# Performance work log

Measured on AMD Instinct MI355X. Metric: run time of the kernel, lower is better.

Reference implementation:

```python
import jax, jax.numpy as jnp
import numpy as np

B, D_IMG, D_NUM, P = 16384, 2048, 256, 128

def setup_inputs() -> dict:
    key = jax.random.key(0)
    ks = jax.random.split(key, 12)
    s = lambda d: 1.0 / np.sqrt(d)
    return {
        "img_feat": jax.random.normal(ks[0], (B, D_IMG), jnp.float32),
        "num_feat": jax.random.normal(ks[1], (B, D_NUM), jnp.float32),
        "Wi1": jax.random.uniform(ks[2], (D_IMG, P), jnp.float32, -s(D_IMG), s(D_IMG)),
        "bi1": jax.random.uniform(ks[3], (P,), jnp.float32, -s(D_IMG), s(D_IMG)),
        "Wi2": jax.random.uniform(ks[4], (P, P), jnp.float32, -s(P), s(P)),
        "bi2": jax.random.uniform(ks[5], (P,), jnp.float32, -s(P), s(P)),
        "Wn1": jax.random.uniform(ks[6], (D_NUM, P), jnp.float32, -s(D_NUM), s(D_NUM)),
        "bn1": jax.random.uniform(ks[7], (P,), jnp.float32, -s(D_NUM), s(D_NUM)),
        "Wn2": jax.random.uniform(ks[8], (P, P), jnp.float32, -s(P), s(P)),
        "bn2": jax.random.uniform(ks[9], (P,), jnp.float32, -s(P), s(P)),
        "log_temp": jnp.asarray(np.log(0.1), jnp.float32),
    }

def _mlp(x, W1, b1, W2, b2):
    h = jax.nn.relu(x @ W1 + b1)
    return h @ W2 + b2

def _l2norm(x, eps=1e-12):
    # matches F.normalize(dim=1): x / max(||x||, eps)
    n = jnp.sqrt(jnp.sum(x * x, axis=1, keepdims=True))
    return x / jnp.maximum(n, eps)

def reference(img_feat, num_feat, Wi1, bi1, Wi2, bi2, Wn1, bn1, Wn2, bn2, log_temp):
    temp = jnp.exp(log_temp)
    ip = _l2norm(_mlp(img_feat, Wi1, bi1, Wi2, bi2))  # [B, P]
    npj = _l2norm(_mlp(num_feat, Wn1, bn1, Wn2, bn2))  # [B, P]
    logits = (ip @ npj.T) / temp                        # [B, B]
    # symmetric cross-entropy with labels = arange(B): targets on the diagonal
    lse_rows = jax.nn.logsumexp(logits, axis=1)  # i2n
    lse_cols = jax.nn.logsumexp(logits, axis=0)  # n2i (logits.T rows)
    diag = jnp.diagonal(logits)
    loss_i2n = jnp.mean(lse_rows - diag)
    loss_n2i = jnp.mean(lse_cols - diag)
    return (loss_i2n + loss_n2i) * 0.5
```

## Files before the change

### kernel.cpp

```cpp
#include <hip/hip_runtime.h>
#include <hip/hip_bf16.h>

typedef __bf16 bf16_t;
typedef __bf16 bf16x8 __attribute__((ext_vector_type(8)));
typedef float f32x4 __attribute__((ext_vector_type(4)));

#define NB 16384
#define NSPLIT 16
#define CG (NB / NSPLIT)
#define BNT 64
#define NT (CG / BNT)

__device__ inline bf16x8 ld8(const bf16_t* p) { return *(const bf16x8*)p; }

__device__ inline void gload_lds16(const bf16_t* g, bf16_t* l) {
  __builtin_amdgcn_global_load_lds(
      (const __attribute__((address_space(1))) unsigned int*)g,
      (__attribute__((address_space(3))) unsigned int*)l, 16, 0, 0);
}

__global__ void prep(const float* __restrict__ img, const float* __restrict__ num,
                     const float* __restrict__ Wi1, const float* __restrict__ Wn1,
                     const float* __restrict__ Wi2, const float* __restrict__ Wn2,
                     bf16_t* __restrict__ imgb, bf16_t* __restrict__ numb,
                     bf16_t* __restrict__ Wi1t, bf16_t* __restrict__ Wn1t,
                     bf16_t* __restrict__ Wi2t, bf16_t* __restrict__ Wn2t,
                     float* __restrict__ lossacc, int nimg, int nnum) {
  int b = blockIdx.x;
  if (b < nimg) {
    int base = b * 8192;
#pragma unroll
    for (int i = 0; i < 4; i++) {
      int e = base + (threadIdx.x + i * 256) * 8;
      int row = e >> 11, k = e & 2047;
      float4 f0 = *(const float4*)(img + e);
      float4 f1 = *(const float4*)(img + e + 4);
      bf16x8 v;
      v[0]=(bf16_t)f0.x; v[1]=(bf16_t)f0.y; v[2]=(bf16_t)f0.z; v[3]=(bf16_t)f0.w;
      v[4]=(bf16_t)f1.x; v[5]=(bf16_t)f1.y; v[6]=(bf16_t)f1.z; v[7]=(bf16_t)f1.w;
      *(bf16x8*)(imgb + (size_t)row * 2048 + (k ^ ((row & 7) << 3))) = v;
    }
    return;
  }
  b -= nimg;
  if (b < nnum) {
    int base = b * 8192;
#pragma unroll
    for (int i = 0; i < 4; i++) {
      int e = base + (threadIdx.x + i * 256) * 8;
      int row = e >> 8, k = e & 255;
      float4 f0 = *(const float4*)(num + e);
      float4 f1 = *(const float4*)(num + e + 4);
      bf16x8 v;
      v[0]=(bf16_t)f0.x; v[1]=(bf16_t)f0.y; v[2]=(bf16_t)f0.z; v[3]=(bf16_t)f0.w;
      v[4]=(bf16_t)f1.x; v[5]=(bf16_t)f1.y; v[6]=(bf16_t)f1.z; v[7]=(bf16_t)f1.w;
      *(bf16x8*)(numb + (size_t)row * 256 + (k ^ ((row & 7) << 3))) = v;
    }
    return;
  }
  b -= nnum;
  if (b < 1280) {
    int idx = b * 256 + threadIdx.x;
    if (idx < 262144) { int k = idx >> 7, n = idx & 127;
      Wi1t[n * 2048 + (k ^ ((n & 7) << 3))] = (bf16_t)Wi1[idx]; return; }
    idx -= 262144;
    if (idx < 32768) { int k = idx >> 7, n = idx & 127;
      Wn1t[n * 256 + (k ^ ((n & 7) << 3))] = (bf16_t)Wn1[idx]; return; }
    idx -= 32768;
    if (idx < 16384) { int k = idx >> 7, n = idx & 127;
      Wi2t[n * 128 + (k ^ ((n & 7) << 3))] = (bf16_t)Wi2[idx]; return; }
    idx -= 16384;
    { int k = idx >> 7, n = idx & 127;
      Wn2t[n * 128 + (k ^ ((n & 7) << 3))] = (bf16_t)Wn2[idx]; }
  } else {
    if (threadIdx.x < 2) lossacc[threadIdx.x] = 0.f;
  }
}

template <bool PRE>
__global__ __launch_bounds__(256, 4) void mlp_fused(
    const bf16_t* __restrict__ imgb, const bf16_t* __restrict__ numb,
    const float* __restrict__ imgf, const float* __restrict__ numf,
    const bf16_t* __restrict__ Wi1t, const bf16_t* __restrict__ Wn1t,
    const bf16_t* __restrict__ Wi2t, const bf16_t* __restrict__ Wn2t,
    const float* __restrict__ bi1, const float* __restrict__ bn1,
    const float* __restrict__ bi2, const float* __restrict__ bn2,
    bf16_t* __restrict__ ipb, bf16_t* __restrict__ npb) {
  __shared__ bf16_t As[32 * 128];
  __shared__ bf16_t Bs[128 * 128];
  __shared__ float rnorm[32];
  const int bid = blockIdx.x;
  const bool isnum = bid >= 512;
  const bf16_t* Xb = isnum ? numb : imgb;
  const float*  Xf = isnum ? numf : imgf;
  const bf16_t* W1 = isnum ? Wn1t : Wi1t;
  const bf16_t* W2 = isnum ? Wn2t : Wi2t;
  const float* b1  = isnum ? bn1 : bi1;
  const float* b2  = isnum ? bn2 : bi2;
  bf16_t* Out = isnum ? npb : ipb;
  const int K = isnum ? 256 : 2048;
  const int t = threadIdx.x, l = t & 63, wid = t >> 6;
  const int wm = wid >> 1, wn = wid & 1;
  const int row0 = (bid & 511) * 32;
  if (t < 32) rnorm[t] = 0.f;

  f32x4 acc[4];
#pragma unroll
  for (int j = 0; j < 4; j++) acc[j] = (f32x4){0.f, 0.f, 0.f, 0.f};

  for (int k0 = 0; k0 < K; k0 += 128) {
    __syncthreads();
#pragma unroll
    for (int i = 0; i < 2; i++) {
      int s = t + i * 256;
      if constexpr (PRE) {
        gload_lds16(Xb + (size_t)(row0 + (s >> 4)) * K + k0 + (s & 15) * 8, As + s * 8);
      } else {
        int r = s >> 4, c = s & 15;
        const float* src = Xf + (size_t)(row0 + r) * K + k0 + c * 8;
        float4 f0 = *(const float4*)(src);
        float4 f1 = *(const float4*)(src + 4);
        bf16x8 v;
        v[0]=(bf16_t)f0.x; v[1]=(bf16_t)f0.y; v[2]=(bf16_t)f0.z; v[3]=(bf16_t)f0.w;
        v[4]=(bf16_t)f1.x; v[5]=(bf16_t)f1.y; v[6]=(bf16_t)f1.z; v[7]=(bf16_t)f1.w;
        *(bf16x8*)(As + r * 128 + ((c ^ (r & 7)) << 3)) = v;
      }
    }
#pragma unroll
    for (int i = 0; i < 8; i++) {
      int s = t + i * 256;
      gload_lds16(W1 + (size_t)(s >> 4) * K + k0 + (s & 15) * 8, Bs + s * 8);
    }
    __syncthreads();
#pragma unroll
    for (int ks = 0; ks < 4; ks++) {
      int r = wm * 16 + (l & 15);
      int c = ks * 4 + (l >> 4);
      bf16x8 a = ld8(As + r * 128 + ((c ^ (r & 7)) << 3));
#pragma unroll
      for (int nt = 0; nt < 4; nt++) {
        int rb = wn * 64 + nt * 16 + (l & 15);
        bf16x8 bfr = ld8(Bs + rb * 128 + ((c ^ (rb & 7)) << 3));
        acc[nt] = __builtin_amdgcn_mfma_f32_16x16x32_bf16(a, bfr, acc[nt], 0, 0, 0);
      }
    }
  }
  __syncthreads();
  {
    int rbase = wm * 16 + ((l >> 4) << 2);
#pragma unroll
    for (int nt = 0; nt < 4; nt++) {
      int col = wn * 64 + nt * 16 + (l & 15);
      float bv = b1[col];
#pragma unroll
      for (int r4 = 0; r4 < 4; r4++) {
        int row = rbase + r4;
        float h = fmaxf(acc[nt][r4] + bv, 0.f);
        As[row * 128 + (col ^ ((row & 7) << 3))] = (bf16_t)h;
      }
    }
  }
#pragma unroll
  for (int i = 0; i < 8; i++) {
    int s = t + i * 256;
    gload_lds16(W2 + (size_t)(s >> 4) * 128 + (s & 15) * 8, Bs + s * 8);
  }
  __syncthreads();
  f32x4 acc2[4];
#pragma unroll
  for (int j = 0; j < 4; j++) acc2[j] = (f32x4){0.f, 0.f, 0.f, 0.f};
#pragma unroll
  for (int ks = 0; ks < 4; ks++) {
    int r = wm * 16 + (l & 15);
    int c = ks * 4 + (l >> 4);
    bf16x8 a = ld8(As + r * 128 + ((c ^ (r & 7)) << 3));
#pragma unroll
    for (int nt = 0; nt < 4; nt++) {
      int rb = wn * 64 + nt * 16 + (l & 15);
      bf16x8 bfr = ld8(Bs + rb * 128 + ((c ^ (rb & 7)) << 3));
      acc2[nt] = __builtin_amdgcn_mfma_f32_16x16x32_bf16(a, bfr, acc2[nt], 0, 0, 0);
    }
  }
  float vv[4][4];
#pragma unroll
  for (int nt = 0; nt < 4; nt++) {
    int col = wn * 64 + nt * 16 + (l & 15);
    float bv = b2[col];
#pragma unroll
    for (int r4 = 0; r4 < 4; r4++) vv[nt][r4] = acc2[nt][r4] + bv;
  }
#pragma unroll
  for (int r4 = 0; r4 < 4; r4++) {
    float p = 0.f;
#pragma unroll
    for (int nt = 0; nt < 4; nt++) p += vv[nt][r4] * vv[nt][r4];
    p += __shfl_xor(p, 1); p += __shfl_xor(p, 2);
    p += __shfl_xor(p, 4); p += __shfl_xor(p, 8);
    if ((l & 15) == 0) atomicAdd(&rnorm[wm * 16 + ((l >> 4) << 2) + r4], p);
  }
  __syncthreads();
#pragma unroll
  for (int r4 = 0; r4 < 4; r4++) {
    int rl = wm * 16 + ((l >> 4) << 2) + r4;
    float sc = 1.f / fmaxf(sqrtf(rnorm[rl]), 1e-12f);
#pragma unroll
    for (int nt = 0; nt < 4; nt++) {
      int col = wn * 64 + nt * 16 + (l & 15);
      int swcol = col ^ ((rl & 7) << 3);
      Out[(size_t)(row0 + rl) * 128 + swcol] = (bf16_t)(vv[nt][r4] * sc);
    }
  }
}

__global__ __launch_bounds__(512, 6) void logits_split(
    const bf16_t* __restrict__ IP, const bf16_t* __restrict__ NP,
    const float* __restrict__ log_temp, float* __restrict__ rowpart,
    float* __restrict__ colpart, float* __restrict__ diag) {
  __shared__ bf16_t BsAll[2 * BNT * 128];
  __shared__ float colred[CG];
  __shared__ float rowred[2][128];
  int bid = blockIdx.x;
  int sw = (bid & 7) * (128 * NSPLIT / 8) + (bid >> 3);
  int bm = sw >> 4, g = sw & (NSPLIT - 1);
  const int t = threadIdx.x, l = t & 63, wid = t >> 6;
  const int wm = wid >> 1, wn = wid & 1;
  const float invt = __expf(-log_temp[0]);
  const float kk = invt * 1.44269504088896f;

  for (int i = t; i < CG; i += 512) colred[i] = 0.f;
#pragma unroll
  for (int i = 0; i < 4; i++) {
    int s = t + i * 512;
    gload_lds16(IP + (size_t)bm * (128 * 128) + s * 8, BsAll + s * 8);
  }
  __syncthreads();
  bf16x8 af[2][4];
#pragma unroll
  for (int mt = 0; mt < 2; mt++) {
    int r = wm * 32 + mt * 16 + (l & 15);
#pragma unroll
    for (int ks = 0; ks < 4; ks++) {
      int c = ks * 4 + (l >> 4);
      af[mt][ks] = ld8(BsAll + r * 128 + ((c ^ (r & 7)) << 3));
    }
  }
  __syncthreads();
#pragma unroll
  for (int i = 0; i < 2; i++) {
    int s = t + i * 512;
    gload_lds16(NP + (size_t)(g * CG) * 128 + s * 8, BsAll + s * 8);
  }
  __syncthreads();

  f32x4 racc[2];
  racc[0] = (f32x4){0.f, 0.f, 0.f, 0.f};
  racc[1] = (f32x4){0.f, 0.f, 0.f, 0.f};

#pragma unroll 1
  for (int tl = 0; tl < NT; tl++) {
    bf16_t* Bsc = BsAll + (tl & 1) * (BNT * 128);
    if (tl + 1 < NT) {
      bf16_t* Bsn = BsAll + ((tl + 1) & 1) * (BNT * 128);
      const bf16_t* src = NP + (size_t)(g * CG + (tl + 1) * BNT) * 128;
#pragma unroll
      for (int i = 0; i < 2; i++) {
        int s = t + i * 512;
        gload_lds16(src + s * 8, Bsn + s * 8);
      }
    }
    f32x4 acc[2][2];
#pragma unroll
    for (int i = 0; i < 2; i++)
#pragma unroll
      for (int j = 0; j < 2; j++) acc[i][j] = (f32x4){0.f, 0.f, 0.f, 0.f};
#pragma unroll
    for (int ks = 0; ks < 4; ks++) {
      int c = ks * 4 + (l >> 4);
      bf16x8 b[2];
#pragma unroll
      for (int nt = 0; nt < 2; nt++) {
        int rb = wn * 32 + nt * 16 + (l & 15);
        b[nt] = ld8(Bsc + rb * 128 + ((c ^ (rb & 7)) << 3));
      }
#pragma unroll
      for (int mt = 0; mt < 2; mt++) {
        acc[mt][0] = __builtin_amdgcn_mfma_f32_16x16x32_bf16(af[mt][ks], b[0], acc[mt][0], 0, 0, 0);
        acc[mt][1] = __builtin_amdgcn_mfma_f32_16x16x32_bf16(af[mt][ks], b[1], acc[mt][1], 0, 0, 0);
      }
    }
    const int colbase = g * CG + tl * BNT;
    if ((colbase >> 7) == bm) {
#pragma unroll
      for (int mt = 0; mt < 2; mt++)
#pragma unroll
        for (int nt = 0; nt < 2; nt++)
#pragma unroll
          for (int r4 = 0; r4 < 4; r4++) {
            int gr = bm * 128 + wm * 32 + mt * 16 + ((l >> 4) << 2) + r4;
            int gc = colbase + wn * 32 + nt * 16 + (l & 15);
            if (gr == gc) diag[gr] = acc[mt][nt][r4] * invt;
          }
    }
#pragma unroll
    for (int mt = 0; mt < 2; mt++)
#pragma unroll
      for (int nt = 0; nt < 2; nt++) {
        f32x4 y = acc[mt][nt] * kk - kk;
#pragma unroll
        for (int r4 = 0; r4 < 4; r4++) acc[mt][nt][r4] = __builtin_amdgcn_exp2f(y[r4]);
      }
#pragma unroll
    for (int mt = 0; mt < 2; mt++) racc[mt] += acc[mt][0] + acc[mt][1];
#pragma unroll
    for (int nt = 0; nt < 2; nt++) {
      f32x4 cv = acc[0][nt] + acc[1][nt];
      float cs = (cv[0] + cv[1]) + (cv[2] + cv[3]);
      cs += __shfl_xor(cs, 16); cs += __shfl_xor(cs, 32);
      if (l < 16) atomicAdd(&colred[tl * BNT + wn * 32 + nt * 16 + l], cs);
    }
    __syncthreads();
  }
#pragma unroll
  for (int mt = 0; mt < 2; mt++)
#pragma unroll
    for (int r4 = 0; r4 < 4; r4++) {
      float rs = racc[mt][r4];
      rs += __shfl_xor(rs, 1); rs += __shfl_xor(rs, 2);
      rs += __shfl_xor(rs, 4); rs += __shfl_xor(rs, 8);
      if ((l & 15) == 0)
        rowred[wn][wm * 32 + mt * 16 + ((l >> 4) << 2) + r4] = rs;
    }
  __syncthreads();
  if (t < 128)
    rowpart[(size_t)g * NB + bm * 128 + t] = rowred[0][t] + rowred[1][t];
  for (int c = t; c < CG; c += 512)
    colpart[(size_t)bm * NB + g * CG + c] = colred[c];
}

__global__ void finalize(const float* __restrict__ rowpart, const float* __restrict__ colpart,
                         const float* __restrict__ diag, const float* __restrict__ log_temp,
                         float* __restrict__ lossacc, float* __restrict__ out) {
  int i = blockIdx.x * 64 + threadIdx.x;
  float rsum = 0.f, csum = 0.f;
#pragma unroll
  for (int g = 0; g < NSPLIT; g++) rsum += rowpart[(size_t)g * NB + i];
#pragma unroll 16
  for (int b = 0; b < 128; b++) csum += colpart[(size_t)b * NB + i];
  float v = 0.5f * (logf(rsum) + logf(csum)) - diag[i];
  for (int m = 1; m < 64; m <<= 1) v += __shfl_xor(v, m);
  if (threadIdx.x == 0) {
    atomicAdd(lossacc, v);
    __threadfence();
    unsigned n = atomicAdd((unsigned*)(lossacc + 1), 1u);
    if (n == gridDim.x - 1) {
      float tot = atomicAdd(lossacc, 0.f);
      out[0] = tot / (float)NB + __expf(-log_temp[0]);
    }
  }
}

extern "C" void kernel_launch(void* const* d_in, const int* in_sizes, int n_in,
                              void* d_out, int out_size, void* d_ws, size_t ws_size,
                              hipStream_t stream) {
  const float* img = (const float*)d_in[0];
  const float* num = (const float*)d_in[1];
  const float* Wi1 = (const float*)d_in[2];
  const float* bi1 = (const float*)d_in[3];
  const float* Wi2 = (const float*)d_in[4];
  const float* bi2 = (const float*)d_in[5];
  const float* Wn1 = (const float*)d_in[6];
  const float* bn1 = (const float*)d_in[7];
  const float* Wn2 = (const float*)d_in[8];
  const float* bn2 = (const float*)d_in[9];
  const float* log_temp = (const float*)d_in[10];
  float* out = (float*)d_out;

  char* w = (char*)d_ws;
  bf16_t* ipb  = (bf16_t*)(w);
  bf16_t* npb  = (bf16_t*)(w + (4u << 20));
  float* colpart = (float*)(w + (8u << 20));

  const size_t need_big = (90ull << 20) + (64ull << 10) + 8;
  const bool big = ws_size >= need_big;

  bf16_t *imgb, *numb, *Wi1t, *Wn1t, *Wi2t, *Wn2t;
  float *rowpart, *diag, *lossacc;
  if (big) {
    imgb = (bf16_t*)(w + (16u << 20));
    numb = (bf16_t*)(w + (80u << 20));
    Wi1t = (bf16_t*)(w + (88u << 20));
    Wn1t = (bf16_t*)(w + (88u << 20) + (512u << 10));
    Wi2t = (bf16_t*)(w + (88u << 20) + (576u << 10));
    Wn2t = (bf16_t*)(w + (88u << 20) + (640u << 10));
    rowpart = (float*)(w + (89u << 20));
    diag    = (float*)(w + (90u << 20));
    lossacc = (float*)(w + (90u << 20) + (64u << 10));
  } else {
    imgb = numb = (bf16_t*)w;
    Wi1t = (bf16_t*)(w + (16u << 20));
    Wn1t = (bf16_t*)(w + (16u << 20) + (512u << 10));
    Wi2t = (bf16_t*)(w + (16u << 20) + (576u << 10));
    Wn2t = (bf16_t*)(w + (16u << 20) + (640u << 10));
    rowpart = (float*)(w + (16u << 20));
    diag    = (float*)(w + (17u << 20));
    lossacc = (float*)(w + (17u << 20) + (64u << 10));
  }

  const int nimg = big ? 4096 : 0, nnum = big ? 512 : 0;
  prep<<<dim3(nimg + nnum + 1280 + 1), 256, 0, stream>>>(
      img, num, Wi1, Wn1, Wi2, Wn2, imgb, numb, Wi1t, Wn1t, Wi2t, Wn2t,
      lossacc, nimg, nnum);
  if (big) {
    mlp_fused<true><<<dim3(1024), 256, 0, stream>>>(
        imgb, numb, img, num, Wi1t, Wn1t, Wi2t, Wn2t,
        bi1, bn1, bi2, bn2, ipb, npb);
  } else {
    mlp_fused<false><<<dim3(1024), 256, 0, stream>>>(
        imgb, numb, img, num, Wi1t, Wn1t, Wi2t, Wn2t,
        bi1, bn1, bi2, bn2, ipb, npb);
  }
  logits_split<<<dim3(128 * NSPLIT), 512, 0, stream>>>(ipb, npb, log_temp,
                                                       rowpart, colpart, diag);
  finalize<<<dim3(NB / 64), 64, 0, stream>>>(rowpart, colpart, diag, log_temp,
                                             lossacc, out);
}
```

Baseline: 412.5 us.

## Drop input pre-conversion pass and double-buffer the MLP K loop

Removes the separate prep pass that converted img/num features to swizzled bf16 in a workspace, so mlp_fused now always reads fp32 inputs and converts them in registers. The first-layer K loop is double-buffered in LDS, issuing the next tile's loads before computing the current one, with one barrier per iteration. The aim is to cut the extra full read/write of the 128 MB image tensor and to overlap loads with MFMA. LDS use roughly doubles, so launch bounds drop to 2 blocks per CU, and logits_split launch bounds also change from 6 to 4.

```diff
diff --git a/kernel.cpp b/kernel.cpp
--- a/kernel.cpp
+++ b/kernel.cpp
@@ -19,46 +19,12 @@
       (__attribute__((address_space(3))) unsigned int*)l, 16, 0, 0);
 }
 
-__global__ void prep(const float* __restrict__ img, const float* __restrict__ num,
-                     const float* __restrict__ Wi1, const float* __restrict__ Wn1,
+__global__ void prep(const float* __restrict__ Wi1, const float* __restrict__ Wn1,
                      const float* __restrict__ Wi2, const float* __restrict__ Wn2,
-                     bf16_t* __restrict__ imgb, bf16_t* __restrict__ numb,
                      bf16_t* __restrict__ Wi1t, bf16_t* __restrict__ Wn1t,
                      bf16_t* __restrict__ Wi2t, bf16_t* __restrict__ Wn2t,
-                     float* __restrict__ lossacc, int nimg, int nnum) {
+                     float* __restrict__ lossacc) {
   int b = blockIdx.x;
-  if (b < nimg) {
-    int base = b * 8192;
-#pragma unroll
-    for (int i = 0; i < 4; i++) {
-      int e = base + (threadIdx.x + i * 256) * 8;
-      int row = e >> 11, k = e & 2047;
-      float4 f0 = *(const float4*)(img + e);
-      float4 f1 = *(const float4*)(img + e + 4);
-      bf16x8 v;
-      v[0]=(bf16_t)f0.x; v[1]=(bf16_t)f0.y; v[2]=(bf16_t)f0.z; v[3]=(bf16_t)f0.w;
-      v[4]=(bf16_t)f1.x; v[5]=(bf16_t)f1.y; v[6]=(bf16_t)f1.z; v[7]=(bf16_t)f1.w;
-      *(bf16x8*)(imgb + (size_t)row * 2048 + (k ^ ((row & 7) << 3))) = v;
-    }
-    return;
-  }
-  b -= nimg;
-  if (b < nnum) {
-    int base = b * 8192;
-#pragma unroll
-    for (int i = 0; i < 4; i++) {
-      int e = base + (threadIdx.x + i * 256) * 8;
-      int row = e >> 8, k = e & 255;
-      float4 f0 = *(const float4*)(num + e);
-      float4 f1 = *(const float4*)(num + e + 4);
-      bf16x8 v;
-      v[0]=(bf16_t)f0.x; v[1]=(bf16_t)f0.y; v[2]=(bf16_t)f0.z; v[3]=(bf16_t)f0.w;
-      v[4]=(bf16_t)f1.x; v[5]=(bf16_t)f1.y; v[6]=(bf16_t)f1.z; v[7]=(bf16_t)f1.w;
-      *(bf16x8*)(numb + (size_t)row * 256 + (k ^ ((row & 7) << 3))) = v;
-    }
-    return;
-  }
-  b -= nnum;
   if (b < 1280) {
     int idx = b * 256 + threadIdx.x;
     if (idx < 262144) { int k = idx >> 7, n = idx & 127;
@@ -77,21 +43,17 @@
   }
 }
 
-template <bool PRE>
-__global__ __launch_bounds__(256, 4) void mlp_fused(
-    const bf16_t* __restrict__ imgb, const bf16_t* __restrict__ numb,
+__global__ __launch_bounds__(256, 2) void mlp_fused(
     const float* __restrict__ imgf, const float* __restrict__ numf,
     const bf16_t* __restrict__ Wi1t, const bf16_t* __restrict__ Wn1t,
     const bf16_t* __restrict__ Wi2t, const bf16_t* __restrict__ Wn2t,
     const float* __restrict__ bi1, const float* __restrict__ bn1,
     const float* __restrict__ bi2, const float* __restrict__ bn2,
     bf16_t* __restrict__ ipb, bf16_t* __restrict__ npb) {
-  __shared__ bf16_t As[32 * 128];
-  __shared__ bf16_t Bs[128 * 128];
-  __shared__ float rnorm[32];
+  __shared__ bf16_t As[2][32 * 128];
+  __shared__ bf16_t Bs[2][128 * 128];
   const int bid = blockIdx.x;
   const bool isnum = bid >= 512;
-  const bf16_t* Xb = isnum ? numb : imgb;
   const float*  Xf = isnum ? numf : imgf;
   const bf16_t* W1 = isnum ? Wn1t : Wi1t;
   const bf16_t* W2 = isnum ? Wn2t : Wi2t;
@@ -99,53 +61,70 @@
   const float* b2  = isnum ? bn2 : bi2;
   bf16_t* Out = isnum ? npb : ipb;
   const int K = isnum ? 256 : 2048;
+  const int NK = K >> 7;
   const int t = threadIdx.x, l = t & 63, wid = t >> 6;
   const int wm = wid >> 1, wn = wid & 1;
   const int row0 = (bid & 511) * 32;
-  if (t < 32) rnorm[t] = 0.f;
-
-  f32x4 acc[4];
-#pragma unroll
-  for (int j = 0; j < 4; j++) acc[j] = (f32x4){0.f, 0.f, 0.f, 0.f};
-
-  for (int k0 = 0; k0 < K; k0 += 128) {
-    __syncthreads();
+
+  auto stageA = [&](int kk, int buf) {
 #pragma unroll
     for (int i = 0; i < 2; i++) {
       int s = t + i * 256;
-      if constexpr (PRE) {
-        gload_lds16(Xb + (size_t)(row0 + (s >> 4)) * K + k0 + (s & 15) * 8, As + s * 8);
-      } else {
-        int r = s >> 4, c = s & 15;
-        const float* src = Xf + (size_t)(row0 + r) * K + k0 + c * 8;
-        float4 f0 = *(const float4*)(src);
-        float4 f1 = *(const float4*)(src + 4);
-        bf16x8 v;
-        v[0]=(bf16_t)f0.x; v[1]=(bf16_t)f0.y; v[2]=(bf16_t)f0.z; v[3]=(bf16_t)f0.w;
-        v[4]=(bf16_t)f1.x; v[5]=(bf16_t)f1.y; v[6]=(bf16_t)f1.z; v[7]=(bf16_t)f1.w;
-        *(bf16x8*)(As + r * 128 + ((c ^ (r & 7)) << 3)) = v;
-      }
-    }
+      int r = s >> 4, c = s & 15;
+      const float* src = Xf + (size_t)(row0 + r) * K + kk * 128 + c * 8;
+      float4 f0 = *(const float4*)(src);
+      float4 f1 = *(const float4*)(src + 4);
+      bf16x8 v;
+      v[0]=(bf16_t)f0.x; v[1]=(bf16_t)f0.y; v[2]=(bf16_t)f0.z; v[3]=(bf16_t)f0.w;
+      v[4]=(bf16_t)f1.x; v[5]=(bf16_t)f1.y; v[6]=(bf16_t)f1.z; v[7]=(bf16_t)f1.w;
+      *(bf16x8*)(As[buf] + r * 128 + ((c ^ (r & 7)) << 3)) = v;
+    }
+  };
+  auto stageB = [&](int kk, int buf) {
 #pragma unroll
     for (int i = 0; i < 8; i++) {
       int s = t + i * 256;
-      gload_lds16(W1 + (size_t)(s >> 4) * K + k0 + (s & 15) * 8, Bs + s * 8);
-    }
-    __syncthreads();
+      gload_lds16(W1 + (size_t)(s >> 4) * K + kk * 128 + (s & 15) * 8,
+                  Bs[buf] + s * 8);
+    }
+  };
+
+  f32x4 acc[4];
+#pragma unroll
+  for (int j = 0; j < 4; j++) acc[j] = (f32x4){0.f, 0.f, 0.f, 0.f};
+
+  stageA(0, 0);
+  stageB(0, 0);
+  __syncthreads();
+
+  for (int kk = 0; kk < NK; kk++) {
+    const int cur = kk & 1;
+    if (kk + 1 < NK) {
+      stageA(kk + 1, cur ^ 1);
+      stageB(kk + 1, cur ^ 1);
+    }
 #pragma unroll
     for (int ks = 0; ks < 4; ks++) {
       int r = wm * 16 + (l & 15);
       int c = ks * 4 + (l >> 4);
-      bf16x8 a = ld8(As + r * 128 + ((c ^ (r & 7)) << 3));
+      bf16x8 a = ld8(As[cur] + r * 128 + ((c ^ (r & 7)) << 3));
 #pragma unroll
       for (int nt = 0; nt < 4; nt++) {
         int rb = wn * 64 + nt * 16 + (l & 15);
-        bf16x8 bfr = ld8(Bs + rb * 128 + ((c ^ (rb & 7)) << 3));
+        bf16x8 bfr = ld8(Bs[cur] + rb * 128 + ((c ^ (rb & 7)) << 3));
         acc[nt] = __builtin_amdgcn_mfma_f32_16x16x32_bf16(a, bfr, acc[nt], 0, 0, 0);
       }
     }
-  }
-  __syncthreads();
+    __syncthreads();
+  }
+
+  float* rnorm = (float*)As[1];
+#pragma unroll
+  for (int i = 0; i < 8; i++) {
+    int s = t + i * 256;
+    gload_lds16(W2 + (size_t)(s >> 4) * 128 + (s & 15) * 8, Bs[0] + s * 8);
+  }
+  if (t < 32) rnorm[t] = 0.f;
   {
     int rbase = wm * 16 + ((l >> 4) << 2);
 #pragma unroll
@@ -156,16 +135,12 @@
       for (int r4 = 0; r4 < 4; r4++) {
         int row = rbase + r4;
         float h = fmaxf(acc[nt][r4] + bv, 0.f);
-        As[row * 128 + (col ^ ((row & 7) << 3))] = (bf16_t)h;
-      }
-    }
-  }
-#pragma unroll
-  for (int i = 0; i < 8; i++) {
-    int s = t + i * 256;
-    gload_lds16(W2 + (size_t)(s >> 4) * 128 + (s & 15) * 8, Bs + s * 8);
-  }
-  __syncthreads();
+        As[0][row * 128 + (col ^ ((row & 7) << 3))] = (bf16_t)h;
+      }
+    }
+  }
+  __syncthreads();
+
   f32x4 acc2[4];
 #pragma unroll
   for (int j = 0; j < 4; j++) acc2[j] = (f32x4){0.f, 0.f, 0.f, 0.f};
@@ -173,11 +148,11 @@
   for (int ks = 0; ks < 4; ks++) {
     int r = wm * 16 + (l & 15);
     int c = ks * 4 + (l >> 4);
-    bf16x8 a = ld8(As + r * 128 + ((c ^ (r & 7)) << 3));
+    bf16x8 a = ld8(As[0] + r * 128 + ((c ^ (r & 7)) << 3));
 #pragma unroll
     for (int nt = 0; nt < 4; nt++) {
       int rb = wn * 64 + nt * 16 + (l & 15);
-      bf16x8 bfr = ld8(Bs + rb * 128 + ((c ^ (rb & 7)) << 3));
+      bf16x8 bfr = ld8(Bs[0] + rb * 128 + ((c ^ (rb & 7)) << 3));
       acc2[nt] = __builtin_amdgcn_mfma_f32_16x16x32_bf16(a, bfr, acc2[nt], 0, 0, 0);
     }
   }
@@ -212,7 +187,7 @@
   }
 }
 
-__global__ __launch_bounds__(512, 6) void logits_split(
+__global__ __launch_bounds__(512, 4) void logits_split(
     const bf16_t* __restrict__ IP, const bf16_t* __restrict__ NP,
     const float* __restrict__ log_temp, float* __restrict__ rowpart,
     float* __restrict__ colpart, float* __restrict__ diag) {
@@ -379,46 +354,18 @@
   bf16_t* ipb  = (bf16_t*)(w);
   bf16_t* npb  = (bf16_t*)(w + (4u << 20));
   float* colpart = (float*)(w + (8u << 20));
-
-  const size_t need_big = (90ull << 20) + (64ull << 10) + 8;
-  const bool big = ws_size >= need_big;
-
-  bf16_t *imgb, *numb, *Wi1t, *Wn1t, *Wi2t, *Wn2t;
-  float *rowpart, *diag, *lossacc;
-  if (big) {
-    imgb = (bf16_t*)(w + (16u << 20));
-    numb = (bf16_t*)(w + (80u << 20));
-    Wi1t = (bf16_t*)(w + (88u << 20));
-    Wn1t = (bf16_t*)(w + (88u << 20) + (512u << 10));
-    Wi2t = (bf16_t*)(w + (88u << 20) + (576u << 10));
-    Wn2t = (bf16_t*)(w + (88u << 20) + (640u << 10));
-    rowpart = (float*)(w + (89u << 20));
-    diag    = (float*)(w + (90u << 20));
-    lossacc = (float*)(w + (90u << 20) + (64u << 10));
-  } else {
-    imgb = numb = (bf16_t*)w;
-    Wi1t = (bf16_t*)(w + (16u << 20));
-    Wn1t = (bf16_t*)(w + (16u << 20) + (512u << 10));
-    Wi2t = (bf16_t*)(w + (16u << 20) + (576u << 10));
-    Wn2t = (bf16_t*)(w + (16u << 20) + (640u << 10));
-    rowpart = (float*)(w + (16u << 20));
-    diag    = (float*)(w + (17u << 20));
-    lossacc = (float*)(w + (17u << 20) + (64u << 10));
-  }
-
-  const int nimg = big ? 4096 : 0, nnum = big ? 512 : 0;
-  prep<<<dim3(nimg + nnum + 1280 + 1), 256, 0, stream>>>(
-      img, num, Wi1, Wn1, Wi2, Wn2, imgb, numb, Wi1t, Wn1t, Wi2t, Wn2t,
-      lossacc, nimg, nnum);
-  if (big) {
-    mlp_fused<true><<<dim3(1024), 256, 0, stream>>>(
-        imgb, numb, img, num, Wi1t, Wn1t, Wi2t, Wn2t,
-        bi1, bn1, bi2, bn2, ipb, npb);
-  } else {
-    mlp_fused<false><<<dim3(1024), 256, 0, stream>>>(
-        imgb, numb, img, num, Wi1t, Wn1t, Wi2t, Wn2t,
-        bi1, bn1, bi2, bn2, ipb, npb);
-  }
+  bf16_t* Wi1t = (bf16_t*)(w + (16u << 20));
+  bf16_t* Wn1t = (bf16_t*)(w + (16u << 20) + (512u << 10));
+  bf16_t* Wi2t = (bf16_t*)(w + (16u << 20) + (576u << 10));
+  bf16_t* Wn2t = (bf16_t*)(w + (16u << 20) + (640u << 10));
+  float* rowpart = (float*)(w + (16u << 20));
+  float* diag    = (float*)(w + (17u << 20));
+  float* lossacc = (float*)(w + (17u << 20) + (64u << 10));
+
+  prep<<<dim3(1281), 256, 0, stream>>>(Wi1, Wn1, Wi2, Wn2,
+                                       Wi1t, Wn1t, Wi2t, Wn2t, lossacc);
+  mlp_fused<<<dim3(1024), 256, 0, stream>>>(img, num, Wi1t, Wn1t, Wi2t, Wn2t,
+                                            bi1, bn1, bi2, bn2, ipb, npb);
   logits_split<<<dim3(128 * NSPLIT), 512, 0, stream>>>(ipb, npb, log_temp,
                                                        rowpart, colpart, diag);
   finalize<<<dim3(NB / 64), 64, 0, stream>>>(rowpart, colpart, diag, log_temp,
```

New measurement: 356.5 us. 13.6% less time.
